# Optimization experiments

Hardware: AMD Instinct MI355X
Metric: run time of the kernel (lower is better)

The kernel has to match this reference:

```python
import jax, jax.numpy as jnp
import numpy as np

D_MODEL, N_HEADS, D_K, D_FF, N_LAYERS, VOCAB, TGT_LEN = 512, 8, 64, 2048, 4, 32000, 1024
B, S_ENC = 4, 1024


def layernorm(x, g, b, eps=1e-6):
    mu = jnp.mean(x, axis=-1, keepdims=True)
    var = jnp.var(x, axis=-1, keepdims=True)
    return g * (x - mu) / jnp.sqrt(var + eps) + b


def sinusoid_pos_enc(seq_len, d_model):
    # source indexes positions 5 .. tgt_len+4 into the sinusoid table
    pos = jnp.arange(5, seq_len + 5, dtype=jnp.float32)[:, None]
    i = jnp.arange(d_model)
    angle = pos / jnp.power(10000.0, (2 * (i // 2)).astype(jnp.float32) / d_model)
    return jnp.where(i % 2 == 0, jnp.sin(angle), jnp.cos(angle))


def mha(xq, xkv, W, b, g, beta, mask):
    # W: [4, d, d] = (Wq, Wk, Wv, Wo); mask: [B,1,q,k], attend where mask != 0
    Bsz, Sq, _ = xq.shape
    q = (xq @ W[0] + b[0]).reshape(Bsz, Sq, N_HEADS, D_K).transpose(0, 2, 1, 3)
    k = (xkv @ W[1] + b[1]).reshape(Bsz, -1, N_HEADS, D_K).transpose(0, 2, 1, 3)
    v = (xkv @ W[2] + b[2]).reshape(Bsz, -1, N_HEADS, D_K).transpose(0, 2, 1, 3)
    scores = jnp.einsum('bhqd,bhkd->bhqk', q, k) / jnp.sqrt(jnp.float32(D_K))
    scores = jnp.where(mask == 0, jnp.float32(-1e9), scores)
    attn = jax.nn.softmax(scores, axis=-1)
    ctx = jnp.einsum('bhqk,bhkd->bhqd', attn, v).transpose(0, 2, 1, 3).reshape(Bsz, Sq, D_MODEL)
    out = ctx @ W[3] + b[3]
    return layernorm(out + xq, g, beta)


def setup_inputs() -> dict:
    key = jax.random.key(0)
    ks = jax.random.split(key, 8)
    sc = 0.02
    return {
        'dec_inputs': jax.random.randint(ks[0], (B, TGT_LEN), 0, VOCAB, dtype=jnp.int32),
        'enc_inputs': jax.random.randint(ks[1], (B, S_ENC), 0, 50, dtype=jnp.int32),
        'enc_outputs': jax.random.normal(ks[2], (B, S_ENC, D_MODEL), jnp.float32),
        'tgt_emb': jax.random.normal(ks[3], (VOCAB, D_MODEL), jnp.float32) * sc,
        'self_W': jax.random.normal(ks[4], (N_LAYERS, 4, D_MODEL, D_MODEL), jnp.float32) * sc,
        'self_b': jnp.zeros((N_LAYERS, 4, D_MODEL), jnp.float32),
        'enc_W': jax.random.normal(ks[5], (N_LAYERS, 4, D_MODEL, D_MODEL), jnp.float32) * sc,
        'enc_b': jnp.zeros((N_LAYERS, 4, D_MODEL), jnp.float32),
        'ffn_W1': jax.random.normal(ks[6], (N_LAYERS, D_MODEL, D_FF), jnp.float32) * sc,
        'ffn_b1': jnp.zeros((N_LAYERS, D_FF), jnp.float32),
        'ffn_W2': jax.random.normal(ks[7], (N_LAYERS, D_FF, D_MODEL), jnp.float32) * sc,
        'ffn_b2': jnp.zeros((N_LAYERS, D_MODEL), jnp.float32),
        'ln_g': jnp.ones((N_LAYERS, 3, D_MODEL), jnp.float32),
        'ln_b': jnp.zeros((N_LAYERS, 3, D_MODEL), jnp.float32),
    }


def reference(dec_inputs, enc_inputs, enc_outputs, tgt_emb, self_W, self_b, enc_W, enc_b,
              ffn_W1, ffn_b1, ffn_W2, ffn_b2, ln_g, ln_b):
    Bsz, S = dec_inputs.shape
    x = tgt_emb[dec_inputs] + sinusoid_pos_enc(S, D_MODEL)
    # self-attn mask: (pad_k OR lower-triangular) > 0, attend where nonzero (as in source)
    pad_self = (dec_inputs == 0).astype(jnp.float32)[:, None, None, :]      # [B,1,1,S]
    sub = jnp.tril(jnp.ones((S, S), jnp.float32))                           # [S,S]
    self_mask = ((pad_self + sub) > 0).astype(jnp.float32)                  # [B,1,S,S]
    # cross-attn mask: 1 where enc key is PAD; attend where nonzero (as in source)
    cross_mask = (enc_inputs == 0).astype(jnp.float32)[:, None, None, :]    # [B,1,1,S_enc]

    def step(h, p):
        sW, sb, eW, eb, W1, b1, W2, b2, g, bb = p
        h = mha(h, h, sW, sb, g[0], bb[0], self_mask)
        h = mha(h, enc_outputs, eW, eb, g[1], bb[1], cross_mask)
        f = jax.nn.relu(h @ W1 + b1) @ W2 + b2   # Conv1D(k=1) == pointwise dense
        h = layernorm(f + h, g[2], bb[2])
        return h, None

    x, _ = jax.lax.scan(step, x, (self_W, self_b, enc_W, enc_b,
                                  ffn_W1, ffn_b1, ffn_W2, ffn_b2, ln_g, ln_b))
    return x


if __name__ == '__main__':
    out = reference(**setup_inputs())
    print(out.shape, out.dtype)
```

## Files before the change

### kernel.cpp

```cpp
#include <hip/hip_runtime.h>
#include <math.h>

#define D_MODEL 512
#define N_HEADS 8
#define D_KH    64
#define D_FF    2048
#define N_LAYERS 4
#define BSZ     4
#define SEQ     1024

typedef __attribute__((ext_vector_type(8))) __bf16 bf16x8;
typedef __attribute__((ext_vector_type(8))) short  s16x8;
typedef __attribute__((ext_vector_type(4))) float  f32x4;

union BF8 { s16x8 s; bf16x8 b; };

static __device__ inline unsigned short f2b(float f) {
    unsigned u = __float_as_uint(f);
    unsigned r = (u + 0x7fffu + ((u >> 16) & 1u)) >> 16;
    return (unsigned short)r;
}

static __device__ __forceinline__ void async16(const unsigned short* g, unsigned short* l) {
    __builtin_amdgcn_global_load_lds((const __attribute__((address_space(1))) unsigned int*)g,
                                     (__attribute__((address_space(3))) unsigned int*)l, 16, 0, 0);
}

__global__ void embed_kernel(const int* __restrict__ dec, const float* __restrict__ emb,
                             float* __restrict__ x, unsigned short* __restrict__ xb) {
    int idx = blockIdx.x * blockDim.x + threadIdx.x;
    int d  = idx % D_MODEL;
    int bs = idx / D_MODEL;
    int s  = bs % SEQ;
    int tok = dec[bs];
    float pos = (float)(s + 5);
    float e = (float)(d & ~1) * (1.0f / (float)D_MODEL);
    float ang = pos * __expf(-9.210340372f * e);
    float pe = (d & 1) ? __cosf(ang) : __sinf(ang);
    float v = emb[(size_t)tok * D_MODEL + d] + pe;
    x[idx] = v;
    xb[idx] = f2b(v);
}

__global__ void cvt_bf16_kernel(const float* __restrict__ in, unsigned short* __restrict__ outp, int n4) {
    int i = blockIdx.x * blockDim.x + threadIdx.x;
    if (i < n4) {
        float4 f = ((const float4*)in)[i];
        ushort4 h;
        h.x = f2b(f.x); h.y = f2b(f.y); h.z = f2b(f.z); h.w = f2b(f.w);
        ((ushort4*)outp)[i] = h;
    }
}

__global__ void wt_all_kernel(const float* __restrict__ selfW, const float* __restrict__ encW,
                              const float* __restrict__ W1, const float* __restrict__ W2,
                              unsigned short* __restrict__ wtS, unsigned short* __restrict__ wtE,
                              unsigned short* __restrict__ wtF1, unsigned short* __restrict__ wtF2) {
    __shared__ unsigned short Tb[64][72];
    int tile = blockIdx.x;
    int which = tile >> 10, rem = tile & 1023;
    const float* src; unsigned short* dst; int K, N, z, kt, ntile;
    if (which <= 1) {
        src = which ? encW : selfW; dst = which ? wtE : wtS;
        K = 512; N = 512;
        z = rem >> 6; int r2 = rem & 63; kt = r2 & 7; ntile = r2 >> 3;
    } else if (which == 2) {
        src = W1; dst = wtF1; K = 512; N = 2048;
        z = rem >> 8; int r2 = rem & 255; kt = r2 & 7; ntile = r2 >> 3;
    } else {
        src = W2; dst = wtF2; K = 2048; N = 512;
        z = rem >> 8; int r2 = rem & 255; kt = r2 >> 3; ntile = r2 & 7;
    }
    int k0 = kt * 64, n0 = ntile * 64;
    size_t zoff = (size_t)z * K * N;
    src += zoff; dst += zoff;
    int t = threadIdx.x;
    int kr = t & 63, sg = t >> 6;
    const float* sp = src + (size_t)(k0 + kr) * N + n0 + sg * 16;
    #pragma unroll
    for (int j = 0; j < 4; j++) {
        float4 f = *(const float4*)(sp + 4 * j);
        Tb[sg * 16 + 4 * j + 0][kr] = f2b(f.x);
        Tb[sg * 16 + 4 * j + 1][kr] = f2b(f.y);
        Tb[sg * 16 + 4 * j + 2][kr] = f2b(f.z);
        Tb[sg * 16 + 4 * j + 3][kr] = f2b(f.w);
    }
    __syncthreads();
    unsigned short* dp = dst + (size_t)(n0 + kr) * K + k0 + sg * 16;
    *(s16x8*)(dp)     = *(const s16x8*)&Tb[kr][sg * 16];
    *(s16x8*)(dp + 8) = *(const s16x8*)&Tb[kr][sg * 16 + 8];
}

__global__ void prep_kernel(const int* __restrict__ dec, const int* __restrict__ enc,
                            int* __restrict__ cntEnc, int* __restrict__ listEnc,
                            int* __restrict__ anyPadDec) {
    int b = blockIdx.x;
    int lane = threadIdx.x;
    int base = 0;
    for (int c0 = 0; c0 < SEQ; c0 += 64) {
        bool z = (enc[b * SEQ + c0 + lane] == 0);
        unsigned long long mask = __ballot(z);
        int pre = __popcll(mask & ((1ull << lane) - 1ull));
        if (z) listEnc[b * SEQ + base + pre] = c0 + lane;
        base += __popcll(mask);
    }
    if (lane == 0) cntEnc[b] = base;
    for (int c0 = 0; c0 < SEQ; c0 += 64) {
        bool z = (dec[b * SEQ + c0 + lane] == 0);
        unsigned long long mask = __ballot(z);
        if (lane == 0) anyPadDec[b * (SEQ / 64) + (c0 >> 6)] = (mask != 0ull) ? 1 : 0;
    }
}

template<int OUTBF16, int RELU, int QKV>
__launch_bounds__(256, 3)
__global__ void gemm_lds_kernel(const unsigned short* __restrict__ A, const unsigned short* __restrict__ A1,
                                const unsigned short* __restrict__ Wt, const float* __restrict__ bias,
                                void* __restrict__ C_, void* __restrict__ C1, void* __restrict__ C2,
                                int M, int N, int K) {
    __shared__ unsigned short lds[2][12288];
    int m0 = blockIdx.x * 128, n0;
    if (QKV) {
        int j = blockIdx.y >> 3;
        n0 = (int)(blockIdx.y & 7) * 64;
        Wt += (size_t)j * (D_MODEL * D_MODEL);
        bias += j * D_MODEL;
        if (j) A = A1;
        if (j == 1) C_ = C1; else if (j == 2) C_ = C2;
    } else n0 = blockIdx.y * 64;

    int t = threadIdx.x, w = t >> 6, lane = t & 63;
    int g = lane >> 4, c = lane & 15;
    int l3 = lane >> 3, l7 = lane & 7;
    int srcoff = 8 * (l7 ^ l3);

    const unsigned short* Abase = A  + (size_t)m0 * K;
    const unsigned short* Bbase = Wt + (size_t)n0 * K;

    f32x4 acc[2][4];
    #pragma unroll
    for (int mi = 0; mi < 2; mi++)
        #pragma unroll
        for (int nj = 0; nj < 4; nj++) acc[mi][nj] = (f32x4){0.f, 0.f, 0.f, 0.f};

#define STAGE(BUF, KT) do {                                                         \
        unsigned short* Lb_ = &lds[BUF][0];                                         \
        int k0_ = (KT) * 64;                                                        \
        _Pragma("unroll")                                                           \
        for (int i_ = 0; i_ < 4; i_++) {                                            \
            int q_ = w * 4 + i_;                                                    \
            async16(Abase + (size_t)(q_ * 8 + l3) * K + k0_ + srcoff, Lb_ + q_ * 512); \
        }                                                                           \
        _Pragma("unroll")                                                           \
        for (int i_ = 0; i_ < 2; i_++) {                                            \
            int q_ = w * 2 + i_;                                                    \
            async16(Bbase + (size_t)(q_ * 8 + l3) * K + k0_ + srcoff, Lb_ + 8192 + q_ * 512); \
        }                                                                           \
    } while (0)

    int nt = K >> 6;
    STAGE(0, 0);
    __syncthreads();
    for (int kt = 0; kt < nt; kt++) {
        int cur = kt & 1;
        if (kt + 1 < nt) STAGE(cur ^ 1, kt + 1);
        const unsigned short* Lb = &lds[cur][0];
        BF8 a[2][2], b[2][4];
        #pragma unroll
        for (int kk = 0; kk < 2; kk++) {
            int xo = (kk * 32 + g * 8) ^ ((c & 7) * 8);
            #pragma unroll
            for (int mi = 0; mi < 2; mi++)
                a[kk][mi].s = *(const s16x8*)&Lb[(w * 32 + mi * 16 + c) * 64 + xo];
            #pragma unroll
            for (int nj = 0; nj < 4; nj++)
                b[kk][nj].s = *(const s16x8*)&Lb[8192 + (nj * 16 + c) * 64 + xo];
        }
        #pragma unroll
        for (int kk = 0; kk < 2; kk++)
            #pragma unroll
            for (int mi = 0; mi < 2; mi++)
                #pragma unroll
                for (int nj = 0; nj < 4; nj++)
                    acc[mi][nj] = __builtin_amdgcn_mfma_f32_16x16x32_bf16(a[kk][mi].b, b[kk][nj].b, acc[mi][nj], 0, 0, 0);
        __syncthreads();
    }
#undef STAGE

    #pragma unroll
    for (int mi = 0; mi < 2; mi++) {
        #pragma unroll
        for (int nj = 0; nj < 4; nj++) {
            #pragma unroll
            for (int r = 0; r < 4; r++) {
                int row = m0 + w * 32 + mi * 16 + g * 4 + r;
                int col = n0 + nj * 16 + c;
                float v = acc[mi][nj][r] + bias[col];
                if (RELU) v = fmaxf(v, 0.0f);
                if (OUTBF16) ((unsigned short*)C_)[(size_t)row * N + col] = f2b(v);
                else         ((float*)C_)[(size_t)row * N + col] = v;
            }
        }
    }
}

template<int OUTBF16, int RELU>
__launch_bounds__(256, 2)
__global__ void gemm128_kernel(const unsigned short* __restrict__ A,
                               const unsigned short* __restrict__ Wt, const float* __restrict__ bias,
                               void* __restrict__ C_, int M, int N, int K) {
    __shared__ unsigned short lds[2][16384];
    int m0 = blockIdx.x * 128, n0 = blockIdx.y * 128;

    int t = threadIdx.x, w = t >> 6, lane = t & 63;
    int wm = w >> 1, wn = w & 1;
    int g = lane >> 4, c = lane & 15;
    int l3 = lane >> 3, l7 = lane & 7;
    int srcoff = 8 * (l7 ^ l3);

    const unsigned short* Abase = A  + (size_t)m0 * K;
    const unsigned short* Bbase = Wt + (size_t)n0 * K;

    f32x4 acc[4][4];
    #pragma unroll
    for (int mi = 0; mi < 4; mi++)
        #pragma unroll
        for (int nj = 0; nj < 4; nj++) acc[mi][nj] = (f32x4){0.f, 0.f, 0.f, 0.f};

#define STAGE128(BUF, KT) do {                                                      \
        unsigned short* Lb_ = &lds[BUF][0];                                         \
        int k0_ = (KT) * 64;                                                        \
        _Pragma("unroll")                                                           \
        for (int i_ = 0; i_ < 4; i_++) {                                            \
            int q_ = w * 4 + i_;                                                    \
            async16(Abase + (size_t)(q_ * 8 + l3) * K + k0_ + srcoff, Lb_ + q_ * 512); \
            async16(Bbase + (size_t)(q_ * 8 + l3) * K + k0_ + srcoff, Lb_ + 8192 + q_ * 512); \
        }                                                                           \
    } while (0)

    int nt = K >> 6;
    STAGE128(0, 0);
    __syncthreads();
    for (int kt = 0; kt < nt; kt++) {
        int cur = kt & 1;
        if (kt + 1 < nt) STAGE128(cur ^ 1, kt + 1);
        const unsigned short* Lb = &lds[cur][0];
        BF8 a[2][4], b[2][4];
        #pragma unroll
        for (int kk = 0; kk < 2; kk++) {
            int xo = (kk * 32 + g * 8) ^ ((c & 7) * 8);
            #pragma unroll
            for (int mi = 0; mi < 4; mi++)
                a[kk][mi].s = *(const s16x8*)&Lb[(wm * 64 + mi * 16 + c) * 64 + xo];
            #pragma unroll
            for (int nj = 0; nj < 4; nj++)
                b[kk][nj].s = *(const s16x8*)&Lb[8192 + (wn * 64 + nj * 16 + c) * 64 + xo];
        }
        #pragma unroll
        for (int kk = 0; kk < 2; kk++)
            #pragma unroll
            for (int mi = 0; mi < 4; mi++)
                #pragma unroll
                for (int nj = 0; nj < 4; nj++)
                    acc[mi][nj] = __builtin_amdgcn_mfma_f32_16x16x32_bf16(a[kk][mi].b, b[kk][nj].b, acc[mi][nj], 0, 0, 0);
        __syncthreads();
    }
#undef STAGE128

    #pragma unroll
    for (int mi = 0; mi < 4; mi++) {
        #pragma unroll
        for (int nj = 0; nj < 4; nj++) {
            #pragma unroll
            for (int r = 0; r < 4; r++) {
                int row = m0 + wm * 64 + mi * 16 + g * 4 + r;
                int col = n0 + wn * 64 + nj * 16 + c;
                float v = acc[mi][nj][r] + bias[col];
                if (RELU) v = fmaxf(v, 0.0f);
                if (OUTBF16) ((unsigned short*)C_)[(size_t)row * N + col] = f2b(v);
                else         ((float*)C_)[(size_t)row * N + col] = v;
            }
        }
    }
}

#define RS 72
template<int MODE>
__global__ void attn_kernel(const unsigned short* __restrict__ Q, const unsigned short* __restrict__ K,
                            const unsigned short* __restrict__ V, const int* __restrict__ ids,
                            const int* __restrict__ list, const int* __restrict__ cnt,
                            const int* __restrict__ anyPad,
                            unsigned short* __restrict__ O_, int Sq, int Sk) {
    __shared__ unsigned short Kl[64][RS];
    __shared__ unsigned short Vt[64][RS];
    __shared__ unsigned short Ps[4][16][RS];
    __shared__ short act[16];
    __shared__ int nActS;

    int blk = blockIdx.x;
    int qt, bh;
    if (MODE) {
        int hi = blk >> 8, pair = blk & 255;
        bh = pair >> 3;
        int qtp = pair & 7;
        qt = hi ? (15 - qtp) : qtp;
    } else {
        qt = blk & 15;
        bh = blk >> 4;
    }
    int h = bh % N_HEADS;
    int b = bh / N_HEADS;
    int qbase = qt * 64;
    int t = threadIdx.x;
    int w = t >> 6, lane = t & 63;
    int g = lane >> 4, c = lane & 15;

    BF8 qf[2];
    {
        int qrow = qbase + w * 16 + c;
        const unsigned short* qp = Q + ((size_t)(b * Sq + qrow)) * D_MODEL + h * D_KH;
        qf[0].s = *(const s16x8*)(qp + 8 * g);
        qf[1].s = *(const s16x8*)(qp + 8 * g + 32);
    }

    int nk = 0;
    bool gathered = false;
    if (!MODE) {
        nk = cnt[b];
        gathered = (nk > 0);
    }

    if (t == 0) {
        int n = 0;
        if (MODE) {
            for (int kt2 = 0; kt2 < (Sk >> 6); kt2++)
                if (kt2 <= qt || anyPad[b * (Sk >> 6) + kt2]) act[n++] = (short)kt2;
        } else {
            int tt = gathered ? ((nk + 63) >> 6) : (Sk >> 6);
            for (int kt2 = 0; kt2 < tt; kt2++) act[n++] = (short)kt2;
        }
        nActS = n;
    }
    __syncthreads();
    int nAct = nActS;

    float m[4], l[4];
    f32x4 Oacc[4];
    #pragma unroll
    for (int r = 0; r < 4; r++) { m[r] = -INFINITY; l[r] = 0.0f; }
    #pragma unroll
    for (int ds = 0; ds < 4; ds++) Oacc[ds] = (f32x4){0.f, 0.f, 0.f, 0.f};

    s16x8 kreg0, kreg1, vreg0, vreg1;
    int kr0 = t >> 3,        ks0 = t & 7;
    int kr1 = (t + 256) >> 3, ks1 = (t + 256) & 7;

#define LOADT(KT) do {                                                                \
        int k0_ = (KT) * 64;                                                          \
        int krow0 = k0_ + kr0, krow1 = k0_ + kr1;                                     \
        if (gathered) {                                                               \
            krow0 = list[b * Sk + (krow0 < nk ? krow0 : nk - 1)];                     \
            krow1 = list[b * Sk + (krow1 < nk ? krow1 : nk - 1)];                     \
        }                                                                             \
        kreg0 = *(const s16x8*)(K + ((size_t)(b * Sk + krow0)) * D_MODEL + h * D_KH + ks0 * 8); \
        kreg1 = *(const s16x8*)(K + ((size_t)(b * Sk + krow1)) * D_MODEL + h * D_KH + ks1 * 8); \
        int li = k0_ + lane, vrow = li;                                               \
        if (gathered) vrow = list[b * Sk + (li < nk ? li : nk - 1)];                  \
        const unsigned short* vp = V + ((size_t)(b * Sk + vrow)) * D_MODEL + h * D_KH + w * 16; \
        vreg0 = *(const s16x8*)(vp);                                                  \
        vreg1 = *(const s16x8*)(vp + 8);                                              \
    } while (0)

    LOADT(act[0]);
    for (int i = 0; i < nAct; i++) {
        int k0 = (int)act[i] * 64;
        __syncthreads();
        *(s16x8*)&Kl[kr0][ks0 * 8] = kreg0;
        *(s16x8*)&Kl[kr1][ks1 * 8] = kreg1;
        #pragma unroll
        for (int j = 0; j < 8; j++) Vt[w * 16 + j][lane] = ((unsigned short*)&vreg0)[j];
        #pragma unroll
        for (int j = 0; j < 8; j++) Vt[w * 16 + 8 + j][lane] = ((unsigned short*)&vreg1)[j];
        __syncthreads();
        if (i + 1 < nAct) LOADT(act[i + 1]);

        f32x4 S[4];
        #pragma unroll
        for (int sub = 0; sub < 4; sub++) {
            BF8 b0, b1;
            b0.s = *(const s16x8*)&Kl[sub * 16 + c][8 * g];
            b1.s = *(const s16x8*)&Kl[sub * 16 + c][8 * g + 32];
            f32x4 s = (f32x4){0.f, 0.f, 0.f, 0.f};
            s = __builtin_amdgcn_mfma_f32_16x16x32_bf16(qf[0].b, b0.b, s, 0, 0, 0);
            s = __builtin_amdgcn_mfma_f32_16x16x32_bf16(qf[1].b, b1.b, s, 0, 0, 0);
            S[sub] = s;
        }

        #pragma unroll
        for (int sub = 0; sub < 4; sub++) {
            int k = k0 + sub * 16 + c;
            bool pad;
            if (MODE) pad = (ids[b * Sk + k] == 0);
            else      pad = gathered ? (k < nk) : false;
            #pragma unroll
            for (int r = 0; r < 4; r++) {
                bool att;
                if (MODE) {
                    int qrow = qbase + w * 16 + g * 4 + r;
                    att = pad || (k <= qrow);
                } else att = pad;
                S[sub][r] = att ? S[sub][r] * 0.125f : -1e9f;
            }
        }

        #pragma unroll
        for (int r = 0; r < 4; r++) {
            float mx = fmaxf(fmaxf(S[0][r], S[1][r]), fmaxf(S[2][r], S[3][r]));
            #pragma unroll
            for (int o = 8; o > 0; o >>= 1) mx = fmaxf(mx, __shfl_xor(mx, o));
            float mn = fmaxf(m[r], mx);
            float sc = __expf(m[r] - mn);
            float lsum = 0.f;
            #pragma unroll
            for (int sub = 0; sub < 4; sub++) {
                float p = __expf(S[sub][r] - mn);
                S[sub][r] = p;
                lsum += p;
            }
            #pragma unroll
            for (int o = 8; o > 0; o >>= 1) lsum += __shfl_xor(lsum, o);
            l[r] = l[r] * sc + lsum;
            m[r] = mn;
            #pragma unroll
            for (int ds = 0; ds < 4; ds++) Oacc[ds][r] *= sc;
        }

        #pragma unroll
        for (int sub = 0; sub < 4; sub++)
            #pragma unroll
            for (int r = 0; r < 4; r++)
                Ps[w][g * 4 + r][sub * 16 + c] = f2b(S[sub][r]);

        #pragma unroll
        for (int kk = 0; kk < 2; kk++) {
            BF8 pa;
            pa.s = *(const s16x8*)&Ps[w][c][8 * g + kk * 32];
            #pragma unroll
            for (int ds = 0; ds < 4; ds++) {
                BF8 vb;
                vb.s = *(const s16x8*)&Vt[ds * 16 + c][8 * g + kk * 32];
                Oacc[ds] = __builtin_amdgcn_mfma_f32_16x16x32_bf16(pa.b, vb.b, Oacc[ds], 0, 0, 0);
            }
        }
    }
#undef LOADT

    #pragma unroll
    for (int r = 0; r < 4; r++) {
        float inv = 1.0f / l[r];
        int qrow = qbase + w * 16 + g * 4 + r;
        unsigned short* op = O_ + ((size_t)(b * Sq + qrow)) * D_MODEL + h * D_KH;
        #pragma unroll
        for (int ds = 0; ds < 4; ds++)
            op[ds * 16 + c] = f2b(Oacc[ds][r] * inv);
    }
}

template<int WRITEB>
__global__ void ln_residual_kernel(const float* __restrict__ f, const float* __restrict__ h,
                                   const float* __restrict__ g, const float* __restrict__ bb,
                                   float* __restrict__ out, unsigned short* __restrict__ outb) {
    int row  = blockIdx.x * 4 + threadIdx.x / 64;
    int lane = threadIdx.x % 64;
    const float* fr = f + (size_t)row * D_MODEL;
    const float* hr = h + (size_t)row * D_MODEL;
    float v[8];
    float s = 0.f;
    #pragma unroll
    for (int i = 0; i < 8; i++) {
        v[i] = fr[lane + i * 64] + hr[lane + i * 64];
        s += v[i];
    }
    #pragma unroll
    for (int o = 32; o > 0; o >>= 1) s += __shfl_xor(s, o);
    float mu = s * (1.0f / 512.0f);
    float ss = 0.f;
    #pragma unroll
    for (int i = 0; i < 8; i++) { float d = v[i] - mu; ss += d * d; }
    #pragma unroll
    for (int o = 32; o > 0; o >>= 1) ss += __shfl_xor(ss, o);
    float var = ss * (1.0f / 512.0f);
    float inv = 1.0f / sqrtf(var + 1e-6f);
    #pragma unroll
    for (int i = 0; i < 8; i++) {
        int d = lane + i * 64;
        float o2 = g[d] * (v[i] - mu) * inv + bb[d];
        out[(size_t)row * D_MODEL + d] = o2;
        if (WRITEB) outb[(size_t)row * D_MODEL + d] = f2b(o2);
    }
}

extern "C" void kernel_launch(void* const* d_in, const int* in_sizes, int n_in,
                              void* d_out, int out_size, void* d_ws, size_t ws_size,
                              hipStream_t stream) {
    const int*   dec     = (const int*)d_in[0];
    const int*   enc_ids = (const int*)d_in[1];
    const float* enc_out = (const float*)d_in[2];
    const float* emb     = (const float*)d_in[3];
    const float* self_W  = (const float*)d_in[4];
    const float* self_b  = (const float*)d_in[5];
    const float* enc_W   = (const float*)d_in[6];
    const float* enc_b   = (const float*)d_in[7];
    const float* W1      = (const float*)d_in[8];
    const float* b1      = (const float*)d_in[9];
    const float* W2      = (const float*)d_in[10];
    const float* b2      = (const float*)d_in[11];
    const float* ln_g    = (const float*)d_in[12];
    const float* ln_b    = (const float*)d_in[13];
    float* out = (float*)d_out;

    const size_t NTOK = (size_t)BSZ * SEQ;
    float* x  = (float*)d_ws;
    float* bA = x + NTOK * D_MODEL;
    unsigned short* xb   = (unsigned short*)(bA + NTOK * D_MODEL);
    unsigned short* encb = xb + NTOK * D_MODEL;
    unsigned short* bQ = encb + NTOK * D_MODEL;
    unsigned short* bK = bQ + NTOK * D_MODEL;
    unsigned short* bV = bK + NTOK * D_MODEL;
    unsigned short* bD = bV + NTOK * D_MODEL;
    unsigned short* bH = bQ;
    unsigned short* wtS  = bD + NTOK * D_MODEL;
    unsigned short* wtE  = wtS + (size_t)N_LAYERS * 4 * D_MODEL * D_MODEL;
    unsigned short* wtF1 = wtE + (size_t)N_LAYERS * 4 * D_MODEL * D_MODEL;
    unsigned short* wtF2 = wtF1 + (size_t)N_LAYERS * D_MODEL * D_FF;
    int* cntEnc    = (int*)(wtF2 + (size_t)N_LAYERS * D_FF * D_MODEL);
    int* anyPadDec = cntEnc + BSZ;
    int* listEnc   = anyPadDec + BSZ * (SEQ / 64);

    dim3 blk(256);
    embed_kernel<<<dim3((unsigned)(NTOK * D_MODEL / 256)), blk, 0, stream>>>(dec, emb, x, xb);
    cvt_bf16_kernel<<<dim3((unsigned)(NTOK * D_MODEL / 4 / 256)), blk, 0, stream>>>(enc_out, encb, (int)(NTOK * D_MODEL / 4));
    prep_kernel<<<dim3(BSZ), dim3(64), 0, stream>>>(dec, enc_ids, cntEnc, listEnc, anyPadDec);
    wt_all_kernel<<<dim3(4096), blk, 0, stream>>>(self_W, enc_W, W1, W2, wtS, wtE, wtF1, wtF2);

    int M = (int)NTOK;
    dim3 gqkv(M / 128, 24);
    dim3 gp  (M / 128, D_MODEL / 64);
    dim3 gf1 (M / 128, D_FF / 128);
    dim3 gf2 (M / 128, D_MODEL / 64);
    int nAttnBlk = BSZ * N_HEADS * (SEQ / 64);

    const size_t WT = (size_t)D_MODEL * D_MODEL;
    for (int L = 0; L < N_LAYERS; L++) {
        const unsigned short* sWt = wtS + (size_t)L * 4 * WT;
        const unsigned short* eWt = wtE + (size_t)L * 4 * WT;
        const float* sb = self_b + (size_t)L * 4 * D_MODEL;
        const float* eb = enc_b  + (size_t)L * 4 * D_MODEL;
        const float* g  = ln_g   + (size_t)L * 3 * D_MODEL;
        const float* bs = ln_b   + (size_t)L * 3 * D_MODEL;

        gemm_lds_kernel<1,0,1><<<gqkv, blk, 0, stream>>>(xb, xb, sWt, sb, bQ, bK, bV, M, D_MODEL, D_MODEL);
        attn_kernel<1><<<dim3(nAttnBlk), blk, 0, stream>>>(bQ, bK, bV, dec, listEnc, cntEnc, anyPadDec, bD, SEQ, SEQ);
        gemm_lds_kernel<0,0,0><<<gp, blk, 0, stream>>>(bD, nullptr, sWt + 3 * WT, sb + 3 * D_MODEL, bA, nullptr, nullptr, M, D_MODEL, D_MODEL);
        ln_residual_kernel<1><<<dim3(M / 4), blk, 0, stream>>>(bA, x, g + 0 * D_MODEL, bs + 0 * D_MODEL, x, xb);

        gemm_lds_kernel<1,0,1><<<gqkv, blk, 0, stream>>>(xb, encb, eWt, eb, bQ, bK, bV, M, D_MODEL, D_MODEL);
        attn_kernel<0><<<dim3(nAttnBlk), blk, 0, stream>>>(bQ, bK, bV, enc_ids, listEnc, cntEnc, anyPadDec, bD, SEQ, SEQ);
        gemm_lds_kernel<0,0,0><<<gp, blk, 0, stream>>>(bD, nullptr, eWt + 3 * WT, eb + 3 * D_MODEL, bA, nullptr, nullptr, M, D_MODEL, D_MODEL);
        ln_residual_kernel<1><<<dim3(M / 4), blk, 0, stream>>>(bA, x, g + 1 * D_MODEL, bs + 1 * D_MODEL, x, xb);

        gemm128_kernel<1,1><<<gf1, blk, 0, stream>>>(xb, wtF1 + (size_t)L * D_MODEL * D_FF, b1 + (size_t)L * D_FF,    bH, M, D_FF,    D_MODEL);
        gemm_lds_kernel<0,0,0><<<gf2, blk, 0, stream>>>(bH, nullptr, wtF2 + (size_t)L * D_FF * D_MODEL, b2 + (size_t)L * D_MODEL, bA, nullptr, nullptr, M, D_MODEL, D_FF);
        float* lnout = (L == N_LAYERS - 1) ? out : x;
        ln_residual_kernel<1><<<dim3(M / 4), blk, 0, stream>>>(bA, x, g + 2 * D_MODEL, bs + 2 * D_MODEL, lnout, xb);
    }
}
```

Measured before the change: 587.3 us.

## Use 64x64-tile GEMM for N=512 projections and double-buffer attention K/V tiles

Adds a gemm64 kernel with 64x64 output tiles, double-buffered async LDS staging and up to 4 blocks per CU. It replaces the 128x64-tile kernel for the output projections and the FFN down-projection, so those N=512 GEMMs launch twice as many blocks and fill the CUs better. Attention now double-buffers its K/V LDS tiles, writing the next tile after the current compute, which drops one barrier per iteration. The cost is more LDS in attention and less reuse per tile in the smaller GEMM.

```diff
diff --git a/kernel.cpp b/kernel.cpp
--- a/kernel.cpp
+++ b/kernel.cpp
@@ -205,6 +205,86 @@
 }
 
 template<int OUTBF16, int RELU>
+__launch_bounds__(256, 4)
+__global__ void gemm64_kernel(const unsigned short* __restrict__ A,
+                              const unsigned short* __restrict__ Wt, const float* __restrict__ bias,
+                              void* __restrict__ C_, int M, int N, int K) {
+    __shared__ unsigned short lds[2][8192];
+    int m0 = blockIdx.x * 64, n0 = blockIdx.y * 64;
+
+    int t = threadIdx.x, w = t >> 6, lane = t & 63;
+    int wm = w >> 1, wn = w & 1;
+    int g = lane >> 4, c = lane & 15;
+    int l3 = lane >> 3, l7 = lane & 7;
+    int srcoff = 8 * (l7 ^ l3);
+
+    const unsigned short* Abase = A  + (size_t)m0 * K;
+    const unsigned short* Bbase = Wt + (size_t)n0 * K;
+
+    f32x4 acc[2][2];
+    #pragma unroll
+    for (int mi = 0; mi < 2; mi++)
+        #pragma unroll
+        for (int nj = 0; nj < 2; nj++) acc[mi][nj] = (f32x4){0.f, 0.f, 0.f, 0.f};
+
+#define STAGE64(BUF, KT) do {                                                       \
+        unsigned short* Lb_ = &lds[BUF][0];                                         \
+        int k0_ = (KT) * 64;                                                        \
+        _Pragma("unroll")                                                           \
+        for (int i_ = 0; i_ < 2; i_++) {                                            \
+            int q_ = w * 2 + i_;                                                    \
+            async16(Abase + (size_t)(q_ * 8 + l3) * K + k0_ + srcoff, Lb_ + q_ * 512); \
+            async16(Bbase + (size_t)(q_ * 8 + l3) * K + k0_ + srcoff, Lb_ + 4096 + q_ * 512); \
+        }                                                                           \
+    } while (0)
+
+    int nt = K >> 6;
+    STAGE64(0, 0);
+    __syncthreads();
+    for (int kt = 0; kt < nt; kt++) {
+        int cur = kt & 1;
+        if (kt + 1 < nt) STAGE64(cur ^ 1, kt + 1);
+        const unsigned short* Lb = &lds[cur][0];
+        BF8 a[2][2], b[2][2];
+        #pragma unroll
+        for (int kk = 0; kk < 2; kk++) {
+            int xo = (kk * 32 + g * 8) ^ ((c & 7) * 8);
+            #pragma unroll
+            for (int mi = 0; mi < 2; mi++)
+                a[kk][mi].s = *(const s16x8*)&Lb[(wm * 32 + mi * 16 + c) * 64 + xo];
+            #pragma unroll
+            for (int nj = 0; nj < 2; nj++)
+                b[kk][nj].s = *(const s16x8*)&Lb[4096 + (wn * 32 + nj * 16 + c) * 64 + xo];
+        }
+        #pragma unroll
+        for (int kk = 0; kk < 2; kk++)
+            #pragma unroll
+            for (int mi = 0; mi < 2; mi++)
+                #pragma unroll
+                for (int nj = 0; nj < 2; nj++)
+                    acc[mi][nj] = __builtin_amdgcn_mfma_f32_16x16x32_bf16(a[kk][mi].b, b[kk][nj].b, acc[mi][nj], 0, 0, 0);
+        __syncthreads();
+    }
+#undef STAGE64
+
+    #pragma unroll
+    for (int mi = 0; mi < 2; mi++) {
+        #pragma unroll
+        for (int nj = 0; nj < 2; nj++) {
+            #pragma unroll
+            for (int r = 0; r < 4; r++) {
+                int row = m0 + wm * 32 + mi * 16 + g * 4 + r;
+                int col = n0 + wn * 32 + nj * 16 + c;
+                float v = acc[mi][nj][r] + bias[col];
+                if (RELU) v = fmaxf(v, 0.0f);
+                if (OUTBF16) ((unsigned short*)C_)[(size_t)row * N + col] = f2b(v);
+                else         ((float*)C_)[(size_t)row * N + col] = v;
+            }
+        }
+    }
+}
+
+template<int OUTBF16, int RELU>
 __launch_bounds__(256, 2)
 __global__ void gemm128_kernel(const unsigned short* __restrict__ A,
                                const unsigned short* __restrict__ Wt, const float* __restrict__ bias,
@@ -291,8 +371,8 @@
                             const int* __restrict__ list, const int* __restrict__ cnt,
                             const int* __restrict__ anyPad,
                             unsigned short* __restrict__ O_, int Sq, int Sk) {
-    __shared__ unsigned short Kl[64][RS];
-    __shared__ unsigned short Vt[64][RS];
+    __shared__ unsigned short Kl[2][64][RS];
+    __shared__ unsigned short Vt[2][64][RS];
     __shared__ unsigned short Ps[4][16][RS];
     __shared__ short act[16];
     __shared__ int nActS;
@@ -371,25 +451,29 @@
         vreg1 = *(const s16x8*)(vp + 8);                                              \
     } while (0)
 
+#define WRITET(BUF) do {                                                              \
+        *(s16x8*)&Kl[BUF][kr0][ks0 * 8] = kreg0;                                      \
+        *(s16x8*)&Kl[BUF][kr1][ks1 * 8] = kreg1;                                      \
+        _Pragma("unroll")                                                             \
+        for (int j = 0; j < 8; j++) Vt[BUF][w * 16 + j][lane] = ((unsigned short*)&vreg0)[j]; \
+        _Pragma("unroll")                                                             \
+        for (int j = 0; j < 8; j++) Vt[BUF][w * 16 + 8 + j][lane] = ((unsigned short*)&vreg1)[j]; \
+    } while (0)
+
     LOADT(act[0]);
+    WRITET(0);
+    __syncthreads();
     for (int i = 0; i < nAct; i++) {
+        int cur = i & 1;
         int k0 = (int)act[i] * 64;
-        __syncthreads();
-        *(s16x8*)&Kl[kr0][ks0 * 8] = kreg0;
-        *(s16x8*)&Kl[kr1][ks1 * 8] = kreg1;
-        #pragma unroll
-        for (int j = 0; j < 8; j++) Vt[w * 16 + j][lane] = ((unsigned short*)&vreg0)[j];
-        #pragma unroll
-        for (int j = 0; j < 8; j++) Vt[w * 16 + 8 + j][lane] = ((unsigned short*)&vreg1)[j];
-        __syncthreads();
         if (i + 1 < nAct) LOADT(act[i + 1]);
 
         f32x4 S[4];
         #pragma unroll
         for (int sub = 0; sub < 4; sub++) {
             BF8 b0, b1;
-            b0.s = *(const s16x8*)&Kl[sub * 16 + c][8 * g];
-            b1.s = *(const s16x8*)&Kl[sub * 16 + c][8 * g + 32];
+            b0.s = *(const s16x8*)&Kl[cur][sub * 16 + c][8 * g];
+            b1.s = *(const s16x8*)&Kl[cur][sub * 16 + c][8 * g + 32];
             f32x4 s = (f32x4){0.f, 0.f, 0.f, 0.f};
             s = __builtin_amdgcn_mfma_f32_16x16x32_bf16(qf[0].b, b0.b, s, 0, 0, 0);
             s = __builtin_amdgcn_mfma_f32_16x16x32_bf16(qf[1].b, b1.b, s, 0, 0, 0);
@@ -448,12 +532,16 @@
             #pragma unroll
             for (int ds = 0; ds < 4; ds++) {
                 BF8 vb;
-                vb.s = *(const s16x8*)&Vt[ds * 16 + c][8 * g + kk * 32];
+                vb.s = *(const s16x8*)&Vt[cur][ds * 16 + c][8 * g + kk * 32];
                 Oacc[ds] = __builtin_amdgcn_mfma_f32_16x16x32_bf16(pa.b, vb.b, Oacc[ds], 0, 0, 0);
             }
         }
+
+        if (i + 1 < nAct) WRITET(cur ^ 1);
+        __syncthreads();
     }
 #undef LOADT
+#undef WRITET
 
     #pragma unroll
     for (int r = 0; r < 4; r++) {
@@ -545,9 +633,9 @@
 
     int M = (int)NTOK;
     dim3 gqkv(M / 128, 24);
-    dim3 gp  (M / 128, D_MODEL / 64);
+    dim3 gp64(M / 64, D_MODEL / 64);
     dim3 gf1 (M / 128, D_FF / 128);
-    dim3 gf2 (M / 128, D_MODEL / 64);
+    dim3 gf2 (M / 64, D_MODEL / 64);
     int nAttnBlk = BSZ * N_HEADS * (SEQ / 64);
 
     const size_t WT = (size_t)D_MODEL * D_MODEL;
@@ -561,16 +649,16 @@
 
         gemm_lds_kernel<1,0,1><<<gqkv, blk, 0, stream>>>(xb, xb, sWt, sb, bQ, bK, bV, M, D_MODEL, D_MODEL);
         attn_kernel<1><<<dim3(nAttnBlk), blk, 0, stream>>>(bQ, bK, bV, dec, listEnc, cntEnc, anyPadDec, bD, SEQ, SEQ);
-        gemm_lds_kernel<0,0,0><<<gp, blk, 0, stream>>>(bD, nullptr, sWt + 3 * WT, sb + 3 * D_MODEL, bA, nullptr, nullptr, M, D_MODEL, D_MODEL);
+        gemm64_kernel<0,0><<<gp64, blk, 0, stream>>>(bD, sWt + 3 * WT, sb + 3 * D_MODEL, bA, M, D_MODEL, D_MODEL);
         ln_residual_kernel<1><<<dim3(M / 4), blk, 0, stream>>>(bA, x, g + 0 * D_MODEL, bs + 0 * D_MODEL, x, xb);
 
         gemm_lds_kernel<1,0,1><<<gqkv, blk, 0, stream>>>(xb, encb, eWt, eb, bQ, bK, bV, M, D_MODEL, D_MODEL);
         attn_kernel<0><<<dim3(nAttnBlk), blk, 0, stream>>>(bQ, bK, bV, enc_ids, listEnc, cntEnc, anyPadDec, bD, SEQ, SEQ);
-        gemm_lds_kernel<0,0,0><<<gp, blk, 0, stream>>>(bD, nullptr, eWt + 3 * WT, eb + 3 * D_MODEL, bA, nullptr, nullptr, M, D_MODEL, D_MODEL);
+        gemm64_kernel<0,0><<<gp64, blk, 0, stream>>>(bD, eWt + 3 * WT, eb + 3 * D_MODEL, bA, M, D_MODEL, D_MODEL);
         ln_residual_kernel<1><<<dim3(M / 4), blk, 0, stream>>>(bA, x, g + 1 * D_MODEL, bs + 1 * D_MODEL, x, xb);
 
         gemm128_kernel<1,1><<<gf1, blk, 0, stream>>>(xb, wtF1 + (size_t)L * D_MODEL * D_FF, b1 + (size_t)L * D_FF,    bH, M, D_FF,    D_MODEL);
-        gemm_lds_kernel<0,0,0><<<gf2, blk, 0, stream>>>(bH, nullptr, wtF2 + (size_t)L * D_FF * D_MODEL, b2 + (size_t)L * D_MODEL, bA, nullptr, nullptr, M, D_MODEL, D_FF);
+        gemm64_kernel<0,0><<<gf2, blk, 0, stream>>>(bH, wtF2 + (size_t)L * D_FF * D_MODEL, b2 + (size_t)L * D_MODEL, bA, M, D_MODEL, D_FF);
         float* lnout = (L == N_LAYERS - 1) ? out : x;
         ln_residual_kernel<1><<<dim3(M / 4), blk, 0, stream>>>(bA, x, g + 2 * D_MODEL, bs + 2 * D_MODEL, lnout, xb);
     }
```

Measured after the change: 570.8 us, median of 2. 1.03x faster.
